# Kernel optimization log

Measured on AMD Instinct MI355X. Metric: run time of the kernel, lower is better.

## Reference

```python
import jax, jax.numpy as jnp
import numpy as np

KS, STRIDE, DIL = 5, 1, 1
PAD = (KS + (KS - 1) * (DIL - 1) - 1) // 2
EPS = 1e-5


def _unfold_t(x):
    # x: (N, C, T, V) -> (N, C, T_out, KS, V), zero-padded temporal windows
    N, C, T, V = x.shape
    xp = jnp.pad(x, ((0, 0), (0, 0), (PAD, PAD), (0, 0)))
    t_out = (T + 2 * PAD - DIL * (KS - 1) - 1) // STRIDE + 1
    idx = jnp.arange(t_out)[:, None] * STRIDE + jnp.arange(KS)[None, :] * DIL  # (T_out, KS)
    return xp[:, :, idx, :]


def _bn2d(x, g, b):
    # training-mode BatchNorm2d: biased batch stats over (N, T, V)
    mu = jnp.mean(x, axis=(0, 2, 3), keepdims=True)
    var = jnp.var(x, axis=(0, 2, 3), keepdims=True)
    xn = (x - mu) * jax.lax.rsqrt(var + EPS)
    return xn * g[None, :, None, None] + b[None, :, None, None]


def setup_inputs() -> dict:
    key = jax.random.key(0)
    ks = jax.random.split(key, 8)
    N, C, T, V = 64, 64, 128, 25
    R, O = 8, 128
    s = 0.05
    return {
        "x": jax.random.normal(ks[0], (N, C, T, V), jnp.float32),
        "Wv": jax.random.normal(ks[1], (R, C), jnp.float32) * s,
        "bv": jax.random.normal(ks[2], (R,), jnp.float32) * s,
        "Ww": jax.random.normal(ks[3], (KS * KS, KS), jnp.float32) * s,
        "bw": jax.random.normal(ks[4], (KS * KS,), jnp.float32) * s,
        "g_bn": jnp.ones((R,), jnp.float32),
        "b_bn": jnp.zeros((R,), jnp.float32),
        "Wr": jax.random.normal(ks[5], (R, C), jnp.float32) * s,
        "br": jax.random.normal(ks[6], (R,), jnp.float32) * s,
        "g_r": jnp.ones((R,), jnp.float32),
        "b_r": jnp.zeros((R,), jnp.float32),
        "Wo": jax.random.normal(ks[7], (O, R), jnp.float32) * s,
        "bo": jnp.zeros((O,), jnp.float32),
        "g_o": jnp.ones((O,), jnp.float32),
        "b_o": jnp.zeros((O,), jnp.float32),
    }


def reference(x, Wv, bv, Ww, bw, g_bn, b_bn, Wr, br, g_r, b_r, Wo, bo, g_o, b_o):
    N, C, T, V = x.shape
    # convV (1x1) then unfold both x and v
    v0 = jnp.einsum('rc,nctv->nrtv', Wv, x) + bv[None, :, None, None]
    xu = _unfold_t(x)      # (N, C, T, W, V)
    vu = _unfold_t(v0)     # (N, R, T, W, V)
    # mean over channels, move window dim to channel position for convW
    m = jnp.mean(xu, axis=1).transpose(0, 2, 1, 3)  # (N, W, T, V)
    w = jnp.einsum('ow,nwtv->notv', Ww, m) + bw[None, :, None, None]
    weights = jnp.tanh(w.reshape(N, KS, KS, T, V))  # (N, W, W, T, V)
    att = jnp.einsum('nwutv,nctuv->nctv', weights, vu)  # (N, R, T, V)
    # residual 1x1 conv + BN (in_channels != out_channels -> conv path)
    res = _bn2d(jnp.einsum('rc,nctv->nrtv', Wr, x) + br[None, :, None, None], g_r, b_r)
    h = _bn2d(att, g_bn, b_bn) + res
    h = jnp.where(h >= 0, h, 0.1 * h)  # LeakyReLU(0.1)
    out = _bn2d(jnp.einsum('or,nrtv->notv', Wo, h) + bo[None, :, None, None], g_o, b_o)
    return out
```

## Files before the change

### kernel.cpp

```cpp
#include <hip/hip_runtime.h>
#include <math.h>

#define TV 3200
#define NTV 204800
#define NB 800
constexpr float EPSF = 1e-5f;

__device__ inline float fast_tanh(float x){
  float e = __expf(2.f*x);
  return 1.f - 2.f/(e + 1.f);
}

template<int NS>
__device__ inline void write_partials(float (&vals)[NS], float* __restrict__ out, float* lds){
  int lane = threadIdx.x & 63;
  int wid  = threadIdx.x >> 6;
  #pragma unroll
  for (int s = 0; s < NS; ++s){
    float v = vals[s];
    #pragma unroll
    for (int o = 32; o > 0; o >>= 1) v += __shfl_down(v, o);
    if (lane == 0) lds[s*4 + wid] = v;
  }
  __syncthreads();
  if ((int)threadIdx.x < NS){
    out[threadIdx.x*NB + blockIdx.x] = lds[threadIdx.x*4+0] + lds[threadIdx.x*4+1]
                                     + lds[threadIdx.x*4+2] + lds[threadIdx.x*4+3];
  }
}

__global__ __launch_bounds__(256) void k_proj(const float* __restrict__ x,
    const float* __restrict__ Wv, const float* __restrict__ bv,
    const float* __restrict__ Wr, const float* __restrict__ br,
    float* __restrict__ v0, float* __restrict__ r0, float* __restrict__ s,
    float* __restrict__ pr){
  __shared__ float sWv[512], sWr[512], lds[16*4];
  int tid = threadIdx.x;
  for (int i = tid; i < 512; i += 256){ sWv[i] = Wv[i]; sWr[i] = Wr[i]; }
  __syncthreads();
  int p = blockIdx.x*256 + tid;
  int n = p / TV, tv = p - n*TV;
  const float* xp = x + (size_t)n*64*TV + tv;
  float av[8] = {0,0,0,0,0,0,0,0};
  float ar[8] = {0,0,0,0,0,0,0,0};
  float ssum = 0.f;
  #pragma unroll 8
  for (int c = 0; c < 64; ++c){
    float xv = __builtin_nontemporal_load(xp + (size_t)c*TV);
    ssum += xv;
    #pragma unroll
    for (int r = 0; r < 8; ++r){
      av[r] = fmaf(sWv[r*64+c], xv, av[r]);
      ar[r] = fmaf(sWr[r*64+c], xv, ar[r]);
    }
  }
  s[p] = ssum * 0.015625f;
  float* v0p = v0 + (size_t)n*8*TV + tv;
  float* r0p = r0 + (size_t)n*8*TV + tv;
  float vals[16];
  #pragma unroll
  for (int r = 0; r < 8; ++r){
    v0p[(size_t)r*TV] = av[r] + bv[r];
    float rr = ar[r] + br[r];
    r0p[(size_t)r*TV] = rr;
    vals[r] = rr; vals[8+r] = rr*rr;
  }
  write_partials<16>(vals, pr, lds);
}

__global__ __launch_bounds__(256) void k_wat(const float* __restrict__ s,
    const float* __restrict__ Ww, const float* __restrict__ bw,
    const float* __restrict__ v0, float* __restrict__ att, float* __restrict__ patt){
  __shared__ float sWw[125], sbw[25], lds[16*4];
  int tid = threadIdx.x;
  if (tid < 125) sWw[tid] = Ww[tid];
  if (tid < 25)  sbw[tid] = bw[tid];
  __syncthreads();
  int p = blockIdx.x*256 + tid;
  int n = p / TV, tv = p - n*TV;
  int t = tv / 25, v = tv - t*25;
  const float* sn = s + (size_t)n*TV;
  float m[5];
  #pragma unroll
  for (int k = 0; k < 5; ++k){
    int tt = t + k - 2;
    m[k] = (tt >= 0 && tt < 128) ? sn[tt*25 + v] : 0.f;
  }
  float w2[5] = {0.f,0.f,0.f,0.f,0.f};
  #pragma unroll
  for (int w = 0; w < 5; ++w){
    #pragma unroll
    for (int u = 0; u < 5; ++u){
      int o = w*5 + u;
      float wo = sbw[o];
      #pragma unroll
      for (int k = 0; k < 5; ++k) wo = fmaf(sWw[o*5+k], m[k], wo);
      w2[u] += fast_tanh(wo);
    }
  }
  const float* v0n = v0 + (size_t)n*8*TV;
  float a[8] = {0,0,0,0,0,0,0,0};
  #pragma unroll
  for (int u = 0; u < 5; ++u){
    int tt = t + u - 2;
    if (tt >= 0 && tt < 128){
      float wu = w2[u];
      const float* vp = v0n + tt*25 + v;
      #pragma unroll
      for (int r = 0; r < 8; ++r) a[r] = fmaf(wu, vp[(size_t)r*TV], a[r]);
    }
  }
  float* ap = att + (size_t)n*8*TV + tv;
  float vals[16];
  #pragma unroll
  for (int r = 0; r < 8; ++r){
    ap[(size_t)r*TV] = a[r];
    vals[r] = a[r]; vals[8+r] = a[r]*a[r];
  }
  write_partials<16>(vals, patt, lds);
}

__global__ __launch_bounds__(256) void k_bncoef(const float* __restrict__ pr,
    const float* __restrict__ patt,
    const float* __restrict__ g_bn, const float* __restrict__ b_bn,
    const float* __restrict__ g_r, const float* __restrict__ b_r,
    float* __restrict__ coef){
  __shared__ float lds[8];
  int b = blockIdx.x;
  bool isatt = (b >= 8);
  int r = isatt ? b - 8 : b;
  const float* ps = (isatt ? patt : pr) + r*NB;
  const float* pq = (isatt ? patt : pr) + (8+r)*NB;
  float s1 = 0.f, s2 = 0.f;
  for (int i = threadIdx.x; i < NB; i += 256){ s1 += ps[i]; s2 += pq[i]; }
  int lane = threadIdx.x & 63, wid = threadIdx.x >> 6;
  #pragma unroll
  for (int o = 32; o > 0; o >>= 1){ s1 += __shfl_down(s1, o); s2 += __shfl_down(s2, o); }
  if (lane == 0){ lds[wid] = s1; lds[4+wid] = s2; }
  __syncthreads();
  if (threadIdx.x == 0){
    float sum = lds[0]+lds[1]+lds[2]+lds[3];
    float sq  = lds[4]+lds[5]+lds[6]+lds[7];
    float mu  = sum / (float)NTV;
    float var = sq / (float)NTV - mu*mu;
    float g  = isatt ? g_bn[r] : g_r[r];
    float bb = isatt ? b_bn[r] : b_r[r];
    float a = g * rsqrtf(var + EPSF);
    float c = bb - a*mu;
    int base = isatt ? 0 : 16;
    coef[base + r] = a;
    coef[base + 8 + r] = c;
  }
}

__global__ __launch_bounds__(256) void k_h(const float* __restrict__ att,
    const float* __restrict__ r0, const float* __restrict__ coef,
    float* __restrict__ h, float* __restrict__ ph){
  __shared__ float lds[44*4];
  __shared__ float sc[32];
  int tid = threadIdx.x;
  if (tid < 32) sc[tid] = coef[tid];
  __syncthreads();
  int p = blockIdx.x*256 + tid;
  int n = p / TV, tv = p - n*TV;
  const float* ap = att + (size_t)n*8*TV + tv;
  const float* rp = r0  + (size_t)n*8*TV + tv;
  float* hp = h + (size_t)n*8*TV + tv;
  float hv[8];
  #pragma unroll
  for (int r = 0; r < 8; ++r){
    float z = sc[r]*ap[(size_t)r*TV] + sc[8+r] + sc[16+r]*rp[(size_t)r*TV] + sc[24+r];
    hv[r] = (z >= 0.f) ? z : 0.1f*z;
    hp[(size_t)r*TV] = hv[r];
  }
  float vals[44];
  #pragma unroll
  for (int r = 0; r < 8; ++r) vals[r] = hv[r];
  int cnt = 8;
  #pragma unroll
  for (int r = 0; r < 8; ++r){
    #pragma unroll
    for (int r2 = r; r2 < 8; ++r2) vals[cnt++] = hv[r]*hv[r2];
  }
  write_partials<44>(vals, ph, lds);
}

__global__ __launch_bounds__(256) void k_hredfold(const float* __restrict__ ph,
    const float* __restrict__ Wo, const float* __restrict__ bo,
    const float* __restrict__ g_o, const float* __restrict__ b_o,
    float* __restrict__ fold, float* __restrict__ bfold){
  __shared__ float lds[44*4];
  __shared__ float hstat[44];
  __shared__ double muh[8];
  __shared__ double exx[8][8];
  int tid = threadIdx.x, lane = tid & 63, wid = tid >> 6;
  for (int j = 0; j < 44; ++j){
    float s1 = 0.f;
    for (int i = tid; i < NB; i += 256) s1 += ph[j*NB + i];
    #pragma unroll
    for (int o = 32; o > 0; o >>= 1) s1 += __shfl_down(s1, o);
    if (lane == 0) lds[j*4 + wid] = s1;
  }
  __syncthreads();
  if (tid < 44) hstat[tid] = lds[tid*4] + lds[tid*4+1] + lds[tid*4+2] + lds[tid*4+3];
  __syncthreads();
  if (tid < 8) muh[tid] = (double)hstat[tid] / (double)NTV;
  if (tid == 0){
    int cnt = 8;
    for (int r = 0; r < 8; ++r)
      for (int r2 = r; r2 < 8; ++r2){
        double e = (double)hstat[cnt++] / (double)NTV;
        exx[r][r2] = e; exx[r2][r] = e;
      }
  }
  __syncthreads();
  if (tid < 128){
    int o = tid;
    double w[8];
    for (int r = 0; r < 8; ++r) w[r] = (double)Wo[o*8+r];
    double bob = (double)bo[o];
    double mu = bob;
    for (int r = 0; r < 8; ++r) mu += w[r]*muh[r];
    double t = 0.0;
    for (int r = 0; r < 8; ++r)
      for (int r2 = 0; r2 < 8; ++r2) t += w[r]*w[r2]*exx[r][r2];
    double ey2 = t + 2.0*bob*(mu - bob) + bob*bob;
    double var = ey2 - mu*mu;
    double a = (double)g_o[o] / sqrt(var + (double)EPSF);
    for (int r = 0; r < 8; ++r) fold[o*8+r] = (float)(a * w[r]);
    bfold[o] = (float)(a * (bob - mu) + (double)b_o[o]);
  }
}

__global__ __launch_bounds__(256) void k_out(const float* __restrict__ h,
    const float* __restrict__ fold, const float* __restrict__ bfold,
    float* __restrict__ out){
  __shared__ float sW[1024], sB[128];
  int tid = threadIdx.x;
  for (int i = tid; i < 1024; i += 256) sW[i] = fold[i];
  if (tid < 128) sB[tid] = bfold[tid];
  __syncthreads();
  int p = blockIdx.x*256 + tid;
  int n = p / TV, tv = p - n*TV;
  const float* hp = h + (size_t)n*8*TV + tv;
  float hv[8];
  #pragma unroll
  for (int r = 0; r < 8; ++r) hv[r] = hp[(size_t)r*TV];
  float* op = out + (size_t)n*128*TV + tv;
  #pragma unroll 8
  for (int o = 0; o < 128; ++o){
    float y = sB[o];
    #pragma unroll
    for (int r = 0; r < 8; ++r) y = fmaf(sW[o*8+r], hv[r], y);
    __builtin_nontemporal_store(y, op + (size_t)o*TV);
  }
}

extern "C" void kernel_launch(void* const* d_in, const int* in_sizes, int n_in,
                              void* d_out, int out_size, void* d_ws, size_t ws_size,
                              hipStream_t stream){
  const float* x    = (const float*)d_in[0];
  const float* Wv   = (const float*)d_in[1];
  const float* bv   = (const float*)d_in[2];
  const float* Ww   = (const float*)d_in[3];
  const float* bw   = (const float*)d_in[4];
  const float* g_bn = (const float*)d_in[5];
  const float* b_bn = (const float*)d_in[6];
  const float* Wr   = (const float*)d_in[7];
  const float* br   = (const float*)d_in[8];
  const float* g_r  = (const float*)d_in[9];
  const float* b_r  = (const float*)d_in[10];
  const float* Wo   = (const float*)d_in[11];
  const float* bo   = (const float*)d_in[12];
  const float* g_o  = (const float*)d_in[13];
  const float* b_o  = (const float*)d_in[14];

  float* ws = (float*)d_ws;
  size_t off = 0;
  float* v0   = ws + off; off += 1638400;
  float* r0   = ws + off; off += 1638400;
  float* s    = ws + off; off += 204800;
  float* att  = ws + off; off += 1638400;
  float* hbuf = ws + off; off += 1638400;
  float* pr   = ws + off; off += 16*NB;
  float* patt = ws + off; off += 16*NB;
  float* ph   = ws + off; off += 44*NB;
  float* coef = ws + off; off += 32;
  float* fold = ws + off; off += 1024;
  float* bfold= ws + off; off += 128;

  k_proj    <<<NB, 256, 0, stream>>>(x, Wv, bv, Wr, br, v0, r0, s, pr);
  k_wat     <<<NB, 256, 0, stream>>>(s, Ww, bw, v0, att, patt);
  k_bncoef  <<<16, 256, 0, stream>>>(pr, patt, g_bn, b_bn, g_r, b_r, coef);
  k_h       <<<NB, 256, 0, stream>>>(att, r0, coef, hbuf, ph);
  k_hredfold<<<1, 256, 0, stream>>>(ph, Wo, bo, g_o, b_o, fold, bfold);
  k_out     <<<NB, 256, 0, stream>>>(hbuf, fold, bfold, (float*)d_out);
}
```

Measured before the change: 282.9 us.

## Fuse all stages into one persistent kernel with grid barriers and LDS halos

Replaces the six-kernel pipeline with a single persistent kernel of 256 blocks, each owning a 32-timestep slab of one sample. The v0, r0, att and h tensors stay in registers and LDS instead of round-tripping through global memory. Temporal halos are exchanged through small global buffers, and the BN statistics are combined across blocks with atomic-counter grid barriers. This removes launch gaps and intermediate global traffic. In exchange, each block runs 512 threads with large LDS usage, so only 256 blocks are active, and the spin barriers rely on all blocks being co-resident.

Result: slower. 356.0 us (+25.9%).

```diff
diff --git a/kernel.cpp b/kernel.cpp
--- a/kernel.cpp
+++ b/kernel.cpp
@@ -3,7 +3,9 @@
 
 #define TV 3200
 #define NTV 204800
-#define NB 800
+#define NBLK 256
+#define TT 32
+#define SITES 800
 constexpr float EPSF = 1e-5f;
 
 __device__ inline float fast_tanh(float x){
@@ -11,8 +13,23 @@
   return 1.f - 2.f/(e + 1.f);
 }
 
+__device__ inline void grid_barrier(int* bar, int idx){
+  __threadfence();
+  __syncthreads();
+  if (threadIdx.x == 0){
+    __hip_atomic_fetch_add(&bar[idx], 1, __ATOMIC_ACQ_REL, __HIP_MEMORY_SCOPE_AGENT);
+    int iter = 0;
+    while (__hip_atomic_load(&bar[idx], __ATOMIC_ACQUIRE, __HIP_MEMORY_SCOPE_AGENT) < NBLK){
+      if (++iter > (1 << 24)) break;
+    }
+  }
+  __syncthreads();
+}
+
+__global__ void k_init(int* bar){ if (threadIdx.x < 16) bar[threadIdx.x] = 0; }
+
 template<int NS>
-__device__ inline void write_partials(float (&vals)[NS], float* __restrict__ out, float* lds){
+__device__ inline void write_partials8(float (&vals)[NS], float* __restrict__ outp, float* lds){
   int lane = threadIdx.x & 63;
   int wid  = threadIdx.x >> 6;
   #pragma unroll
@@ -20,239 +37,281 @@
     float v = vals[s];
     #pragma unroll
     for (int o = 32; o > 0; o >>= 1) v += __shfl_down(v, o);
-    if (lane == 0) lds[s*4 + wid] = v;
+    if (lane == 0) lds[s*8 + wid] = v;
   }
   __syncthreads();
   if ((int)threadIdx.x < NS){
-    out[threadIdx.x*NB + blockIdx.x] = lds[threadIdx.x*4+0] + lds[threadIdx.x*4+1]
-                                     + lds[threadIdx.x*4+2] + lds[threadIdx.x*4+3];
-  }
-}
-
-__global__ __launch_bounds__(256) void k_proj(const float* __restrict__ x,
+    float t = 0.f;
+    #pragma unroll
+    for (int w = 0; w < 8; ++w) t += lds[threadIdx.x*8 + w];
+    outp[threadIdx.x*NBLK + blockIdx.x] = t;
+  }
+}
+
+__global__ __launch_bounds__(512) void k_fused(
+    const float* __restrict__ x,
     const float* __restrict__ Wv, const float* __restrict__ bv,
+    const float* __restrict__ Ww, const float* __restrict__ bw,
+    const float* __restrict__ g_bn, const float* __restrict__ b_bn,
     const float* __restrict__ Wr, const float* __restrict__ br,
-    float* __restrict__ v0, float* __restrict__ r0, float* __restrict__ s,
-    float* __restrict__ pr){
-  __shared__ float sWv[512], sWr[512], lds[16*4];
-  int tid = threadIdx.x;
-  for (int i = tid; i < 512; i += 256){ sWv[i] = Wv[i]; sWr[i] = Wr[i]; }
-  __syncthreads();
-  int p = blockIdx.x*256 + tid;
-  int n = p / TV, tv = p - n*TV;
-  const float* xp = x + (size_t)n*64*TV + tv;
-  float av[8] = {0,0,0,0,0,0,0,0};
-  float ar[8] = {0,0,0,0,0,0,0,0};
-  float ssum = 0.f;
-  #pragma unroll 8
-  for (int c = 0; c < 64; ++c){
-    float xv = __builtin_nontemporal_load(xp + (size_t)c*TV);
-    ssum += xv;
-    #pragma unroll
-    for (int r = 0; r < 8; ++r){
-      av[r] = fmaf(sWv[r*64+c], xv, av[r]);
-      ar[r] = fmaf(sWr[r*64+c], xv, ar[r]);
-    }
-  }
-  s[p] = ssum * 0.015625f;
-  float* v0p = v0 + (size_t)n*8*TV + tv;
-  float* r0p = r0 + (size_t)n*8*TV + tv;
-  float vals[16];
-  #pragma unroll
-  for (int r = 0; r < 8; ++r){
-    v0p[(size_t)r*TV] = av[r] + bv[r];
-    float rr = ar[r] + br[r];
-    r0p[(size_t)r*TV] = rr;
-    vals[r] = rr; vals[8+r] = rr*rr;
-  }
-  write_partials<16>(vals, pr, lds);
-}
-
-__global__ __launch_bounds__(256) void k_wat(const float* __restrict__ s,
-    const float* __restrict__ Ww, const float* __restrict__ bw,
-    const float* __restrict__ v0, float* __restrict__ att, float* __restrict__ patt){
-  __shared__ float sWw[125], sbw[25], lds[16*4];
-  int tid = threadIdx.x;
+    const float* __restrict__ g_r, const float* __restrict__ b_r,
+    const float* __restrict__ Wo, const float* __restrict__ bo,
+    const float* __restrict__ g_o, const float* __restrict__ b_o,
+    float* __restrict__ out,
+    float* __restrict__ haloV, float* __restrict__ haloS,
+    float* __restrict__ pr, float* __restrict__ patt, float* __restrict__ ph,
+    int* __restrict__ bar)
+{
+  __shared__ float sV[36*25*9];
+  __shared__ float sS[36*25];
+  __shared__ float sWv[512], sWr[512];
+  __shared__ float sWw[125], sbw[25];
+  __shared__ float red[44*8];
+  __shared__ float sc[32];
+  __shared__ float hstat[44];
+  __shared__ float sW[1024], sB[128];
+
+  const int tid = threadIdx.x;
+  const int b = blockIdx.x;
+  const int n = b >> 2, q = b & 3;
+  const int t0 = q*TT;
+  const bool act1 = (tid < SITES - 512);
+
+  if (tid < 512){ sWv[tid] = Wv[tid]; sWr[tid] = Wr[tid]; }
   if (tid < 125) sWw[tid] = Ww[tid];
   if (tid < 25)  sbw[tid] = bw[tid];
   __syncthreads();
-  int p = blockIdx.x*256 + tid;
-  int n = p / TV, tv = p - n*TV;
-  int t = tv / 25, v = tv - t*25;
-  const float* sn = s + (size_t)n*TV;
-  float m[5];
-  #pragma unroll
-  for (int k = 0; k < 5; ++k){
-    int tt = t + k - 2;
-    m[k] = (tt >= 0 && tt < 128) ? sn[tt*25 + v] : 0.f;
-  }
-  float w2[5] = {0.f,0.f,0.f,0.f,0.f};
-  #pragma unroll
-  for (int w = 0; w < 5; ++w){
-    #pragma unroll
-    for (int u = 0; u < 5; ++u){
-      int o = w*5 + u;
-      float wo = sbw[o];
-      #pragma unroll
-      for (int k = 0; k < 5; ++k) wo = fmaf(sWw[o*5+k], m[k], wo);
-      w2[u] += fast_tanh(wo);
-    }
-  }
-  const float* v0n = v0 + (size_t)n*8*TV;
-  float a[8] = {0,0,0,0,0,0,0,0};
-  #pragma unroll
-  for (int u = 0; u < 5; ++u){
-    int tt = t + u - 2;
-    if (tt >= 0 && tt < 128){
-      float wu = w2[u];
-      const float* vp = v0n + tt*25 + v;
-      #pragma unroll
-      for (int r = 0; r < 8; ++r) a[r] = fmaf(wu, vp[(size_t)r*TV], a[r]);
-    }
-  }
-  float* ap = att + (size_t)n*8*TV + tv;
-  float vals[16];
-  #pragma unroll
-  for (int r = 0; r < 8; ++r){
-    ap[(size_t)r*TV] = a[r];
-    vals[r] = a[r]; vals[8+r] = a[r]*a[r];
-  }
-  write_partials<16>(vals, patt, lds);
-}
-
-__global__ __launch_bounds__(256) void k_bncoef(const float* __restrict__ pr,
-    const float* __restrict__ patt,
-    const float* __restrict__ g_bn, const float* __restrict__ b_bn,
-    const float* __restrict__ g_r, const float* __restrict__ b_r,
-    float* __restrict__ coef){
-  __shared__ float lds[8];
-  int b = blockIdx.x;
-  bool isatt = (b >= 8);
-  int r = isatt ? b - 8 : b;
-  const float* ps = (isatt ? patt : pr) + r*NB;
-  const float* pq = (isatt ? patt : pr) + (8+r)*NB;
-  float s1 = 0.f, s2 = 0.f;
-  for (int i = threadIdx.x; i < NB; i += 256){ s1 += ps[i]; s2 += pq[i]; }
-  int lane = threadIdx.x & 63, wid = threadIdx.x >> 6;
-  #pragma unroll
-  for (int o = 32; o > 0; o >>= 1){ s1 += __shfl_down(s1, o); s2 += __shfl_down(s2, o); }
-  if (lane == 0){ lds[wid] = s1; lds[4+wid] = s2; }
-  __syncthreads();
-  if (threadIdx.x == 0){
-    float sum = lds[0]+lds[1]+lds[2]+lds[3];
-    float sq  = lds[4]+lds[5]+lds[6]+lds[7];
-    float mu  = sum / (float)NTV;
-    float var = sq / (float)NTV - mu*mu;
-    float g  = isatt ? g_bn[r] : g_r[r];
-    float bb = isatt ? b_bn[r] : b_r[r];
-    float a = g * rsqrtf(var + EPSF);
-    float c = bb - a*mu;
-    int base = isatt ? 0 : 16;
-    coef[base + r] = a;
-    coef[base + 8 + r] = c;
-  }
-}
-
-__global__ __launch_bounds__(256) void k_h(const float* __restrict__ att,
-    const float* __restrict__ r0, const float* __restrict__ coef,
-    float* __restrict__ h, float* __restrict__ ph){
-  __shared__ float lds[44*4];
-  __shared__ float sc[32];
-  int tid = threadIdx.x;
-  if (tid < 32) sc[tid] = coef[tid];
-  __syncthreads();
-  int p = blockIdx.x*256 + tid;
-  int n = p / TV, tv = p - n*TV;
-  const float* ap = att + (size_t)n*8*TV + tv;
-  const float* rp = r0  + (size_t)n*8*TV + tv;
-  float* hp = h + (size_t)n*8*TV + tv;
-  float hv[8];
-  #pragma unroll
-  for (int r = 0; r < 8; ++r){
-    float z = sc[r]*ap[(size_t)r*TV] + sc[8+r] + sc[16+r]*rp[(size_t)r*TV] + sc[24+r];
-    hv[r] = (z >= 0.f) ? z : 0.1f*z;
-    hp[(size_t)r*TV] = hv[r];
-  }
-  float vals[44];
-  #pragma unroll
-  for (int r = 0; r < 8; ++r) vals[r] = hv[r];
-  int cnt = 8;
-  #pragma unroll
-  for (int r = 0; r < 8; ++r){
-    #pragma unroll
-    for (int r2 = r; r2 < 8; ++r2) vals[cnt++] = hv[r]*hv[r2];
-  }
-  write_partials<44>(vals, ph, lds);
-}
-
-__global__ __launch_bounds__(256) void k_hredfold(const float* __restrict__ ph,
-    const float* __restrict__ Wo, const float* __restrict__ bo,
-    const float* __restrict__ g_o, const float* __restrict__ b_o,
-    float* __restrict__ fold, float* __restrict__ bfold){
-  __shared__ float lds[44*4];
-  __shared__ float hstat[44];
-  __shared__ double muh[8];
-  __shared__ double exx[8][8];
-  int tid = threadIdx.x, lane = tid & 63, wid = tid >> 6;
-  for (int j = 0; j < 44; ++j){
-    float s1 = 0.f;
-    for (int i = tid; i < NB; i += 256) s1 += ph[j*NB + i];
-    #pragma unroll
-    for (int o = 32; o > 0; o >>= 1) s1 += __shfl_down(s1, o);
-    if (lane == 0) lds[j*4 + wid] = s1;
-  }
-  __syncthreads();
-  if (tid < 44) hstat[tid] = lds[tid*4] + lds[tid*4+1] + lds[tid*4+2] + lds[tid*4+3];
-  __syncthreads();
-  if (tid < 8) muh[tid] = (double)hstat[tid] / (double)NTV;
-  if (tid == 0){
+
+  float r0v[2][8], attv[2][8], hv[2][8];
+  #pragma unroll
+  for (int sl = 0; sl < 2; ++sl)
+    #pragma unroll
+    for (int r = 0; r < 8; ++r){ r0v[sl][r] = 0.f; attv[sl][r] = 0.f; hv[sl][r] = 0.f; }
+
+  #pragma unroll
+  for (int sl = 0; sl < 2; ++sl){
+    bool act = (sl == 0) || act1;
+    if (act){
+      int L = tid + sl*512;
+      int tl = L/25, v = L - tl*25;
+      const float* xp = x + (size_t)n*64*TV + (size_t)(t0+tl)*25 + v;
+      float ssum = 0.f;
+      float av[8] = {0,0,0,0,0,0,0,0};
+      float arr[8] = {0,0,0,0,0,0,0,0};
+      #pragma unroll 8
+      for (int c = 0; c < 64; ++c){
+        float xv = xp[(size_t)c*TV];
+        ssum += xv;
+        #pragma unroll
+        for (int r = 0; r < 8; ++r){
+          av[r]  = fmaf(sWv[r*64+c], xv, av[r]);
+          arr[r] = fmaf(sWr[r*64+c], xv, arr[r]);
+        }
+      }
+      float sval = ssum * 0.015625f;
+      sS[(tl+2)*25 + v] = sval;
+      int lb = ((tl+2)*25 + v)*9;
+      #pragma unroll
+      for (int r = 0; r < 8; ++r){
+        sV[lb + r]  = av[r] + bv[r];
+        r0v[sl][r] = arr[r] + br[r];
+      }
+      if (tl < 2){
+        int base = ((b*2 + 0)*2 + tl)*25 + v;
+        haloS[base] = sval;
+        #pragma unroll
+        for (int r = 0; r < 8; ++r) haloV[base*8 + r] = av[r] + bv[r];
+      }
+      if (tl >= TT-2){
+        int base = ((b*2 + 1)*2 + (tl-(TT-2)))*25 + v;
+        haloS[base] = sval;
+        #pragma unroll
+        for (int r = 0; r < 8; ++r) haloV[base*8 + r] = av[r] + bv[r];
+      }
+    }
+  }
+  {
+    float vals[16];
+    #pragma unroll
+    for (int r = 0; r < 8; ++r){
+      vals[r]   = r0v[0][r] + r0v[1][r];
+      vals[8+r] = r0v[0][r]*r0v[0][r] + r0v[1][r]*r0v[1][r];
+    }
+    write_partials8<16>(vals, pr, red);
+  }
+  grid_barrier(bar, 0);
+
+  for (int i = tid; i < 900; i += 512){
+    if (i < 800){
+      int side = i / 400;
+      int j = i - side*400;
+      int t2 = j / 200; int rem = j - t2*200; int v = rem >> 3; int r = rem & 7;
+      if (side == 0){
+        float val = (q > 0) ? haloV[((((b-1)*2+1)*2 + t2)*25 + v)*8 + r] : 0.f;
+        sV[(t2*25 + v)*9 + r] = val;
+      } else {
+        float val = (q < 3) ? haloV[((((b+1)*2+0)*2 + t2)*25 + v)*8 + r] : 0.f;
+        sV[((34+t2)*25 + v)*9 + r] = val;
+      }
+    } else {
+      int j = i - 800;
+      int side = j / 50; int k2 = j - side*50; int t2 = k2/25; int v = k2 - t2*25;
+      if (side == 0){
+        sS[t2*25 + v] = (q > 0) ? haloS[(((b-1)*2+1)*2 + t2)*25 + v] : 0.f;
+      } else {
+        sS[(34+t2)*25 + v] = (q < 3) ? haloS[(((b+1)*2+0)*2 + t2)*25 + v] : 0.f;
+      }
+    }
+  }
+  __syncthreads();
+
+  #pragma unroll
+  for (int sl = 0; sl < 2; ++sl){
+    bool act = (sl == 0) || act1;
+    if (act){
+      int L = tid + sl*512;
+      int tl = L/25, v = L - tl*25;
+      float m[5];
+      #pragma unroll
+      for (int k = 0; k < 5; ++k) m[k] = sS[(tl+k)*25 + v];
+      float w2[5] = {0.f,0.f,0.f,0.f,0.f};
+      #pragma unroll
+      for (int w = 0; w < 5; ++w){
+        #pragma unroll
+        for (int u = 0; u < 5; ++u){
+          int o = w*5 + u;
+          float wo = sbw[o];
+          #pragma unroll
+          for (int k = 0; k < 5; ++k) wo = fmaf(sWw[o*5+k], m[k], wo);
+          w2[u] += fast_tanh(wo);
+        }
+      }
+      #pragma unroll
+      for (int u = 0; u < 5; ++u){
+        float wu = w2[u];
+        int base = ((tl+u)*25 + v)*9;
+        #pragma unroll
+        for (int r = 0; r < 8; ++r) attv[sl][r] = fmaf(wu, sV[base + r], attv[sl][r]);
+      }
+    }
+  }
+  {
+    float vals[16];
+    #pragma unroll
+    for (int r = 0; r < 8; ++r){
+      vals[r]   = attv[0][r] + attv[1][r];
+      vals[8+r] = attv[0][r]*attv[0][r] + attv[1][r]*attv[1][r];
+    }
+    write_partials8<16>(vals, patt, red);
+  }
+  grid_barrier(bar, 1);
+
+  {
+    int g = tid >> 4;
+    int l4 = tid & 15;
+    const float* src = (g < 16) ? (pr + g*NBLK) : (patt + (g-16)*NBLK);
+    float sm = 0.f;
+    for (int i = l4; i < NBLK; i += 16) sm += src[i];
+    #pragma unroll
+    for (int o = 8; o > 0; o >>= 1) sm += __shfl_down(sm, o, 16);
+    if (l4 == 0) red[g] = sm;
+  }
+  __syncthreads();
+  if (tid < 8){
+    int r = tid;
+    float mu_r  = red[r]     / (float)NTV;
+    float var_r = red[8+r]   / (float)NTV - mu_r*mu_r;
+    float ar_ = g_r[r] * rsqrtf(var_r + EPSF);
+    sc[16+r] = ar_; sc[24+r] = b_r[r] - ar_*mu_r;
+    float mu_a  = red[16+r]  / (float)NTV;
+    float var_a = red[24+r]  / (float)NTV - mu_a*mu_a;
+    float aa = g_bn[r] * rsqrtf(var_a + EPSF);
+    sc[r] = aa; sc[8+r] = b_bn[r] - aa*mu_a;
+  }
+  __syncthreads();
+
+  #pragma unroll
+  for (int sl = 0; sl < 2; ++sl){
+    bool act = (sl == 0) || act1;
+    if (act){
+      #pragma unroll
+      for (int r = 0; r < 8; ++r){
+        float z = sc[r]*attv[sl][r] + sc[8+r] + sc[16+r]*r0v[sl][r] + sc[24+r];
+        hv[sl][r] = (z >= 0.f) ? z : 0.1f*z;
+      }
+    }
+  }
+  {
+    float vals[44];
+    #pragma unroll
+    for (int r = 0; r < 8; ++r) vals[r] = hv[0][r] + hv[1][r];
     int cnt = 8;
-    for (int r = 0; r < 8; ++r)
+    #pragma unroll
+    for (int r = 0; r < 8; ++r){
+      #pragma unroll
       for (int r2 = r; r2 < 8; ++r2){
-        double e = (double)hstat[cnt++] / (double)NTV;
-        exx[r][r2] = e; exx[r2][r] = e;
-      }
+        vals[cnt++] = hv[0][r]*hv[0][r2] + hv[1][r]*hv[1][r2];
+      }
+    }
+    write_partials8<44>(vals, ph, red);
+  }
+  grid_barrier(bar, 2);
+
+  {
+    int wid = tid >> 6, lane = tid & 63;
+    for (int s = wid; s < 44; s += 8){
+      float sm = 0.f;
+      for (int i = lane; i < NBLK; i += 64) sm += ph[s*NBLK + i];
+      #pragma unroll
+      for (int o = 32; o > 0; o >>= 1) sm += __shfl_down(sm, o);
+      if (lane == 0) hstat[s] = sm;
+    }
   }
   __syncthreads();
   if (tid < 128){
     int o = tid;
+    double muh[8];
+    #pragma unroll
+    for (int r = 0; r < 8; ++r) muh[r] = (double)hstat[r] / (double)NTV;
     double w[8];
+    #pragma unroll
     for (int r = 0; r < 8; ++r) w[r] = (double)Wo[o*8+r];
     double bob = (double)bo[o];
     double mu = bob;
+    #pragma unroll
     for (int r = 0; r < 8; ++r) mu += w[r]*muh[r];
     double t = 0.0;
-    for (int r = 0; r < 8; ++r)
-      for (int r2 = 0; r2 < 8; ++r2) t += w[r]*w[r2]*exx[r][r2];
+    for (int r = 0; r < 8; ++r){
+      for (int r2 = 0; r2 < 8; ++r2){
+        int lo = (r < r2) ? r : r2, hi = (r < r2) ? r2 : r;
+        int idx = 8 + lo*8 - (lo*(lo-1))/2 + (hi - lo);
+        t += w[r]*w[r2]*((double)hstat[idx] / (double)NTV);
+      }
+    }
     double ey2 = t + 2.0*bob*(mu - bob) + bob*bob;
     double var = ey2 - mu*mu;
     double a = (double)g_o[o] / sqrt(var + (double)EPSF);
-    for (int r = 0; r < 8; ++r) fold[o*8+r] = (float)(a * w[r]);
-    bfold[o] = (float)(a * (bob - mu) + (double)b_o[o]);
-  }
-}
-
-__global__ __launch_bounds__(256) void k_out(const float* __restrict__ h,
-    const float* __restrict__ fold, const float* __restrict__ bfold,
-    float* __restrict__ out){
-  __shared__ float sW[1024], sB[128];
-  int tid = threadIdx.x;
-  for (int i = tid; i < 1024; i += 256) sW[i] = fold[i];
-  if (tid < 128) sB[tid] = bfold[tid];
-  __syncthreads();
-  int p = blockIdx.x*256 + tid;
-  int n = p / TV, tv = p - n*TV;
-  const float* hp = h + (size_t)n*8*TV + tv;
-  float hv[8];
-  #pragma unroll
-  for (int r = 0; r < 8; ++r) hv[r] = hp[(size_t)r*TV];
-  float* op = out + (size_t)n*128*TV + tv;
-  #pragma unroll 8
-  for (int o = 0; o < 128; ++o){
-    float y = sB[o];
-    #pragma unroll
-    for (int r = 0; r < 8; ++r) y = fmaf(sW[o*8+r], hv[r], y);
-    __builtin_nontemporal_store(y, op + (size_t)o*TV);
+    #pragma unroll
+    for (int r = 0; r < 8; ++r) sW[o*8+r] = (float)(a * w[r]);
+    sB[o] = (float)(a * (bob - mu) + (double)b_o[o]);
+  }
+  __syncthreads();
+
+  #pragma unroll
+  for (int sl = 0; sl < 2; ++sl){
+    bool act = (sl == 0) || act1;
+    if (act){
+      int L = tid + sl*512;
+      int tl = L/25, v = L - tl*25;
+      float* op = out + (size_t)n*128*TV + (size_t)(t0+tl)*25 + v;
+      #pragma unroll 8
+      for (int o = 0; o < 128; ++o){
+        float y = sB[o];
+        #pragma unroll
+        for (int r = 0; r < 8; ++r) y = fmaf(sW[o*8+r], hv[sl][r], y);
+        __builtin_nontemporal_store(y, op + (size_t)o*TV);
+      }
+    }
   }
 }
 
@@ -277,22 +336,15 @@
 
   float* ws = (float*)d_ws;
   size_t off = 0;
-  float* v0   = ws + off; off += 1638400;
-  float* r0   = ws + off; off += 1638400;
-  float* s    = ws + off; off += 204800;
-  float* att  = ws + off; off += 1638400;
-  float* hbuf = ws + off; off += 1638400;
-  float* pr   = ws + off; off += 16*NB;
-  float* patt = ws + off; off += 16*NB;
-  float* ph   = ws + off; off += 44*NB;
-  float* coef = ws + off; off += 32;
-  float* fold = ws + off; off += 1024;
-  float* bfold= ws + off; off += 128;
-
-  k_proj    <<<NB, 256, 0, stream>>>(x, Wv, bv, Wr, br, v0, r0, s, pr);
-  k_wat     <<<NB, 256, 0, stream>>>(s, Ww, bw, v0, att, patt);
-  k_bncoef  <<<16, 256, 0, stream>>>(pr, patt, g_bn, b_bn, g_r, b_r, coef);
-  k_h       <<<NB, 256, 0, stream>>>(att, r0, coef, hbuf, ph);
-  k_hredfold<<<1, 256, 0, stream>>>(ph, Wo, bo, g_o, b_o, fold, bfold);
-  k_out     <<<NB, 256, 0, stream>>>(hbuf, fold, bfold, (float*)d_out);
-}
+  float* haloV = ws + off; off += 204800;
+  float* haloS = ws + off; off += 51200;
+  float* pr    = ws + off; off += 16*NBLK;
+  float* patt  = ws + off; off += 16*NBLK;
+  float* ph    = ws + off; off += 44*NBLK;
+  int*   bar   = (int*)(ws + off); off += 16;
+
+  k_init <<<1, 64, 0, stream>>>(bar);
+  k_fused<<<NBLK, 512, 0, stream>>>(x, Wv, bv, Ww, bw, g_bn, b_bn, Wr, br, g_r, b_r,
+                                    Wo, bo, g_o, b_o, (float*)d_out,
+                                    haloV, haloS, pr, patt, ph, bar);
+}
```
